# Performance work log

Measured on AMD Instinct MI355X. Metric: run time of the kernel, lower is better.

The kernel has to match this reference:

```python
import jax, jax.numpy as jnp
import numpy as np


def setup_inputs() -> dict:
    key = jax.random.key(0)
    k1, k2, k3, k4 = jax.random.split(key, 4)
    B, Cin, Cout, N, modes = 16, 128, 128, 8192, 64
    scale = 1.0 / (Cin * Cout)
    x = jax.random.normal(k1, (B, Cin, N), dtype=jnp.float32)
    # spectral weight: [in, out, modes, 2] uniform in [0, scale) like torch.rand * scale
    w_spec = scale * jax.random.uniform(k2, (Cin, Cout, modes, 2), dtype=jnp.float32)
    # Conv1d(kernel=1) weight [out, in] and bias [out] (kaiming-uniform-ish init)
    bound = 1.0 / np.sqrt(Cin)
    w_conv = jax.random.uniform(k3, (Cout, Cin), minval=-bound, maxval=bound, dtype=jnp.float32)
    b_conv = jax.random.uniform(k4, (Cout,), minval=-bound, maxval=bound, dtype=jnp.float32)
    return {"x": x, "w_spec": w_spec, "w_conv": w_conv, "b_conv": b_conv}


def reference(x, w_spec, w_conv, b_conv):
    N = x.shape[-1]
    modes = w_spec.shape[2]
    n_freq = N // 2 + 1
    # Spectral conv: rfft, keep first `modes` coefficients, complex channel mix
    x_ft = jnp.fft.rfft(x)  # [B, Cin, n_freq] complex64
    w_c = w_spec[..., 0] + 1j * w_spec[..., 1]  # [Cin, Cout, modes]
    out_m = jnp.einsum('bim,iom->bom', x_ft[:, :, :modes], w_c)  # [B, Cout, modes]
    out_ft = jnp.pad(out_m, ((0, 0), (0, 0), (0, n_freq - modes)))
    x1 = jnp.fft.irfft(out_ft, n=N)  # [B, Cout, N]
    # 1x1 conv (pointwise channel mix)
    x2 = jnp.einsum('bin,oi->bon', x, w_conv) + b_conv[None, :, None]
    return jax.nn.gelu(x1 + x2, approximate=False)
```

## Files before the change

kernel.cpp:

```cpp
#include <hip/hip_runtime.h>
#include <hip/hip_bf16.h>
#include <math.h>

#define NB    16
#define NCIN  128
#define NCOUT 128
#define NN    8192
#define NMOD  64

typedef short bf16x8 __attribute__((ext_vector_type(8)));
typedef float f32x4  __attribute__((ext_vector_type(4)));

#define MFMA16(a, b, c) __builtin_amdgcn_mfma_f32_16x16x32_bf16((a), (b), (c), 0, 0, 0)

__device__ inline unsigned short f2bf_rne(float f) {
    unsigned u = __float_as_uint(f);
    u += 0x7FFF + ((u >> 16) & 1);
    return (unsigned short)(u >> 16);
}
__device__ inline short f2bf_trunc(float f) {
    return (short)(__float_as_uint(f) >> 16);
}

__global__ __launch_bounds__(256) void k_prep(const float* __restrict__ wc,
                                              const float* __restrict__ wsp,
                                              unsigned short* __restrict__ T,
                                              unsigned short* __restrict__ Tt,
                                              unsigned short* __restrict__ Wcb,
                                              unsigned short* __restrict__ Wpk) {
    const float C = 7.66990393943e-4f;
    if (blockIdx.x < 16) {
        int a = blockIdx.x * 256 + threadIdx.x;
        int k = a >> 6, n0 = (a & 63) * 128;
        for (int j8 = 0; j8 < 16; ++j8) {
            short c8[8], s8[8];
            #pragma unroll
            for (int j = 0; j < 8; ++j) {
                int n = n0 + j8 * 8 + j;
                int ph = (k * n) & (NN - 1);
                float sn, cs; __sincosf((float)ph * C, &sn, &cs);
                c8[j] = (short)f2bf_rne(cs);
                s8[j] = (short)f2bf_rne(-sn);
            }
            *(bf16x8*)(T + (size_t)(2 * k) * NN + n0 + j8 * 8)     = *(bf16x8*)c8;
            *(bf16x8*)(T + (size_t)(2 * k + 1) * NN + n0 + j8 * 8) = *(bf16x8*)s8;
        }
    } else if (blockIdx.x < 48) {
        int n = (blockIdx.x - 16) * 256 + threadIdx.x;
        for (int k4 = 0; k4 < 16; ++k4) {
            short buf[8];
            #pragma unroll
            for (int j = 0; j < 4; ++j) {
                int k = k4 * 4 + j;
                int ph = (n * k) & (NN - 1);
                float sn, cs; __sincosf((float)ph * C, &sn, &cs);
                buf[2 * j]     = (short)f2bf_rne(cs);
                buf[2 * j + 1] = (short)f2bf_rne(-sn);
            }
            *(bf16x8*)(Tt + (size_t)n * 128 + k4 * 8) = *(bf16x8*)buf;
        }
    } else if (blockIdx.x < 112) {
        int j = (blockIdx.x - 48) * 256 + threadIdx.x;
        if (j < NCOUT * NCIN) Wcb[j] = f2bf_rne(wc[j]);
    } else {
        int g2 = (blockIdx.x - 112) * 256 + threadIdx.x;
        int k  = g2 & 63;
        int o  = (g2 >> 6) & 127;
        int ch = g2 >> 13;
        const float s = (k == 0) ? (1.f / NN) : (2.f / NN);
        const float2* wp = (const float2*)wsp;
        unsigned short* wre = Wpk + ((size_t)(k * 2 + 0) * 128 + o) * 256;
        unsigned short* wim = Wpk + ((size_t)(k * 2 + 1) * 128 + o) * 256;
        for (int c = ch * 8; c < ch * 8 + 8; ++c) {
            int i0 = 4 * c;
            short re8[8], im8[8];
            #pragma unroll
            for (int t2 = 0; t2 < 4; ++t2) {
                float2 wv = wp[((size_t)(i0 + t2) * 128 + o) * 64 + k];
                float wr = s * wv.x, wi = s * wv.y;
                re8[2 * t2]     = (short)f2bf_rne(wr);
                re8[2 * t2 + 1] = (short)f2bf_rne(-wi);
                im8[2 * t2]     = (k == 0) ? (short)0 : (short)f2bf_rne(wi);
                im8[2 * t2 + 1] = (k == 0) ? (short)0 : (short)f2bf_rne(wr);
            }
            *(bf16x8*)(wre + c * 8) = *(bf16x8*)re8;
            *(bf16x8*)(wim + c * 8) = *(bf16x8*)im8;
        }
    }
}

__global__ __launch_bounds__(256) void k_dftmm(const float* __restrict__ x,
                                               const unsigned short* __restrict__ T,
                                               float* __restrict__ Cpart) {
    const int mt = blockIdx.x & 63, sp = blockIdx.x >> 6;
    const int w = threadIdx.x >> 6, l = threadIdx.x & 63;
    const int l15 = l & 15, q = l >> 4;
    const int colbase = w * 32;
    __shared__ short As[8192];

    const int sr = threadIdx.x >> 3;
    const int sc = threadIdx.x & 7;
    const float* xrow = x + (size_t)(mt * 32 + sr) * NN + sp * 512 + sc * 16;
    short* wp0 = As + sr * 128 + (((sc * 2    ) ^ (sr & 7)) * 8);
    short* wp1 = As + sr * 128 + (((sc * 2 + 1) ^ (sr & 7)) * 8);

    float4 ra, rb, rc, rd;
#define LOADC(c) { const float* p_ = xrow + (c) * 128;                         \
        ra = *(const float4*)p_;       rb = *(const float4*)(p_ + 4);          \
        rc = *(const float4*)(p_ + 8); rd = *(const float4*)(p_ + 12); }
#define WRITEC(bufi) {                                                          \
        short t0_[8] = { f2bf_trunc(ra.x), f2bf_trunc(ra.y), f2bf_trunc(ra.z), f2bf_trunc(ra.w), \
                         f2bf_trunc(rb.x), f2bf_trunc(rb.y), f2bf_trunc(rb.z), f2bf_trunc(rb.w) }; \
        short t1_[8] = { f2bf_trunc(rc.x), f2bf_trunc(rc.y), f2bf_trunc(rc.z), f2bf_trunc(rc.w), \
                         f2bf_trunc(rd.x), f2bf_trunc(rd.y), f2bf_trunc(rd.z), f2bf_trunc(rd.w) }; \
        *(bf16x8*)(wp0 + (bufi) * 4096) = *(bf16x8*)t0_;                        \
        *(bf16x8*)(wp1 + (bufi) * 4096) = *(bf16x8*)t1_; }

    const unsigned short* Tp0 = T + (size_t)(colbase + l15) * NN + sp * 512 + q * 8;
    const unsigned short* Tp1 = Tp0 + (size_t)16 * NN;

    const int rsw = l15 & 7;

    LOADC(0);
    WRITEC(0);
    __syncthreads();

    f32x4 acc[2][2] = {};
    int buf = 0;
    for (int c = 0; c < 4; ++c) {
        if (c < 3) LOADC(c + 1);
        const short* Ab = As + buf * 4096;
        #pragma unroll
        for (int kk = 0; kk < 4; ++kk) {
            int ce = ((kk * 4 + q) ^ rsw) * 8;
            bf16x8 a0 = *(const bf16x8*)(Ab + l15 * 128 + ce);
            bf16x8 a1 = *(const bf16x8*)(Ab + (16 + l15) * 128 + ce);
            bf16x8 b0 = *(const bf16x8*)(Tp0 + c * 128 + kk * 32);
            bf16x8 b1 = *(const bf16x8*)(Tp1 + c * 128 + kk * 32);
            acc[0][0] = MFMA16(a0, b0, acc[0][0]);
            acc[0][1] = MFMA16(a0, b1, acc[0][1]);
            acc[1][0] = MFMA16(a1, b0, acc[1][0]);
            acc[1][1] = MFMA16(a1, b1, acc[1][1]);
        }
        if (c < 3) {
            WRITEC(buf ^ 1);
            __syncthreads();
            buf ^= 1;
        }
    }
#undef LOADC
#undef WRITEC

    #pragma unroll
    for (int mf = 0; mf < 2; ++mf)
        #pragma unroll
        for (int nf = 0; nf < 2; ++nf) {
            int col  = colbase + nf * 16 + l15;
            int row0 = mt * 32 + mf * 16 + q * 4;
            *(f32x4*)(Cpart + (size_t)sp * 262144 + (size_t)col * 2048 + row0) = acc[mf][nf];
        }
}

__global__ __launch_bounds__(256) void k_reduce(const float* __restrict__ Cpart,
                                                float* __restrict__ Xf) {
    int t = blockIdx.x * 256 + threadIdx.x;
    float s = 0.f;
    #pragma unroll
    for (int sp = 0; sp < 16; ++sp) s += Cpart[(size_t)sp * 262144 + t];
    Xf[t] = s;
}

__global__ __launch_bounds__(64) void k_mixmm(const float* __restrict__ Xf,
                                              const unsigned short* __restrict__ Wpk,
                                              unsigned short* __restrict__ Aspec) {
    const int k = blockIdx.x >> 3, oq = blockIdx.x & 7;
    const int l = threadIdx.x, l15 = l & 15, q = l >> 4;
    f32x4 ar = {}, ai = {};
    const float* xr = Xf + (size_t)(2 * k) * 2048 + l15 * 128;
    const float* xi = xr + 2048;
    const int o = oq * 16 + l15;
    #pragma unroll
    for (int kt = 0; kt < 8; ++kt) {
        int i0 = kt * 16 + q * 4;
        float4 r4 = *(const float4*)(xr + i0);
        float4 i4 = *(const float4*)(xi + i0);
        short a8[8] = { (short)f2bf_rne(r4.x), (short)f2bf_rne(i4.x),
                        (short)f2bf_rne(r4.y), (short)f2bf_rne(i4.y),
                        (short)f2bf_rne(r4.z), (short)f2bf_rne(i4.z),
                        (short)f2bf_rne(r4.w), (short)f2bf_rne(i4.w) };
        bf16x8 a = *(bf16x8*)a8;
        const unsigned short* wb = Wpk + ((size_t)(k * 2) * 128 + o) * 256 + kt * 32 + q * 8;
        bf16x8 bre = *(const bf16x8*)wb;
        bf16x8 bim = *(const bf16x8*)(wb + 32768);
        ar = MFMA16(a, bre, ar);
        ai = MFMA16(a, bim, ai);
    }
    #pragma unroll
    for (int r = 0; r < 4; ++r) {
        int b = q * 4 + r;
        unsigned v = (unsigned)f2bf_rne(ar[r]) | ((unsigned)f2bf_rne(ai[r]) << 16);
        *(unsigned*)(Aspec + ((size_t)b * 128 + o) * 128 + 2 * k) = v;
    }
}

__global__ __launch_bounds__(256) void k_out(const float* __restrict__ x,
                                             const unsigned short* __restrict__ Tt,
                                             const unsigned short* __restrict__ Aspec,
                                             const unsigned short* __restrict__ Wcb,
                                             const float* __restrict__ bias,
                                             float* __restrict__ out) {
    const int b = blockIdx.x >> 7, nt = blockIdx.x & 127;
    const int w = threadIdx.x >> 6, l = threadIdx.x & 63;
    const int l15 = l & 15, q = l >> 4;
    const int wo = w >> 1, wn = w & 1;
    __shared__ short xs[8192];

    const float* xb = x + (size_t)b * 128 * NN + nt * 64;
    #pragma unroll
    for (int it = 0; it < 4; ++it) {
        int unit = it * 256 + threadIdx.x;
        int ipair = unit >> 4, nq = unit & 15;
        int i0 = ipair * 2;
        const float* p0 = xb + (size_t)i0 * NN + nq * 4;
        float4 r0 = *(const float4*)p0;
        float4 r1 = *(const float4*)(p0 + NN);
        float a0[4] = { r0.x, r0.y, r0.z, r0.w };
        float a1[4] = { r1.x, r1.y, r1.z, r1.w };
        #pragma unroll
        for (int j = 0; j < 4; ++j) {
            int n = nq * 4 + j;
            unsigned v = (unsigned)(unsigned short)f2bf_trunc(a0[j])
                       | ((unsigned)(unsigned short)f2bf_trunc(a1[j]) << 16);
            int swz = (n ^ (n >> 2)) & 15;
            int addr = n * 128 + (((i0 >> 3) ^ swz) * 8) + (i0 & 7);
            *(unsigned*)&xs[addr] = v;
        }
    }

    const int obase = wo * 64;
    const int nbase = nt * 64 + wn * 32;
    f32x4 acc[4][2] = {};
    #pragma unroll
    for (int kt = 0; kt < 4; ++kt) {
        bf16x8 bb[2];
        #pragma unroll
        for (int nf = 0; nf < 2; ++nf) {
            int n = nbase + nf * 16 + l15;
            bb[nf] = *(const bf16x8*)(Tt + (size_t)n * 128 + kt * 32 + q * 8);
        }
        const unsigned short* Ap = Aspec + (size_t)b * 16384 + kt * 32 + q * 8;
        #pragma unroll
        for (int mf = 0; mf < 4; ++mf) {
            bf16x8 a = *(const bf16x8*)(Ap + (size_t)(obase + mf * 16 + l15) * 128);
            acc[mf][0] = MFMA16(a, bb[0], acc[mf][0]);
            acc[mf][1] = MFMA16(a, bb[1], acc[mf][1]);
        }
    }
    __syncthreads();
    #pragma unroll
    for (int kt = 0; kt < 4; ++kt) {
        bf16x8 bb[2];
        #pragma unroll
        for (int nf = 0; nf < 2; ++nf) {
            int nl = wn * 32 + nf * 16 + l15;
            int c  = kt * 4 + q;
            int swz = (nl ^ (nl >> 2)) & 15;
            bb[nf] = *(const bf16x8*)&xs[nl * 128 + ((c ^ swz) * 8)];
        }
        const unsigned short* Ap = Wcb + kt * 32 + q * 8;
        #pragma unroll
        for (int mf = 0; mf < 4; ++mf) {
            bf16x8 a = *(const bf16x8*)(Ap + (size_t)(obase + mf * 16 + l15) * 128);
            acc[mf][0] = MFMA16(a, bb[0], acc[mf][0]);
            acc[mf][1] = MFMA16(a, bb[1], acc[mf][1]);
        }
    }
    #pragma unroll
    for (int mf = 0; mf < 4; ++mf)
        #pragma unroll
        for (int nf = 0; nf < 2; ++nf)
            #pragma unroll
            for (int r = 0; r < 4; ++r) {
                int o = obase + mf * 16 + q * 4 + r;
                int n = nbase + nf * 16 + l15;
                float v = acc[mf][nf][r] + bias[o];
                float u = v * v;
                float p = v * fmaf(0.0713548162f, u, 1.5957691216f);
                float e = __expf(-p);
                float g = v * __builtin_amdgcn_rcpf(1.f + e);
                out[((size_t)(b * 128 + o)) * NN + n] = g;
            }
}

extern "C" void kernel_launch(void* const* d_in, const int* in_sizes, int n_in,
                              void* d_out, int out_size, void* d_ws, size_t ws_size,
                              hipStream_t stream) {
    const float* x    = (const float*)d_in[0];
    const float* wsp  = (const float*)d_in[1];
    const float* wc   = (const float*)d_in[2];
    const float* bc   = (const float*)d_in[3];
    float* out = (float*)d_out;

    unsigned short* T   = (unsigned short*)d_ws;
    unsigned short* Tt  = T + (size_t)1048576;
    unsigned short* Wcb = Tt + (size_t)1048576;
    unsigned short* Asp = Wcb + 16384;
    unsigned short* Wpk = Asp + 262144;
    float* Cpart = (float*)(Wpk + (size_t)8388608);
    float* Xf    = Cpart + (size_t)16 * 262144;

    k_prep  <<<240,  256, 0, stream>>>(wc, wsp, T, Tt, Wcb, Wpk);
    k_dftmm <<<1024, 256, 0, stream>>>(x, T, Cpart);
    k_reduce<<<1024, 256, 0, stream>>>(Cpart, Xf);
    k_mixmm <<<512,  64,  0, stream>>>(Xf, Wpk, Asp);
    k_out   <<<2048, 256, 0, stream>>>(x, Tt, Asp, Wcb, bc, out);
}
```

Measured before the change: 197.9 us.

## Transpose DFT partials layout, pre-pack bf16 in reduce, halve output tile

k_dftmm now writes its partial sums in row-major [row][col] scalar stores instead of transposed f32x4 stores. k_reduce converts the summed spectrum to bf16 and stores it already interleaved in the MFMA A-operand order, so k_mixmm can load the operand with one vector load instead of converting floats. k_out uses 32-column tiles with each wave owning 32 output channels, which doubles the block count and halves the shared-memory footprint. The tradeoffs are scattered scalar stores in k_dftmm and k_reduce, and more blocks in k_out that each reload the spectral and conv weights.

```diff
diff --git a/kernel.cpp b/kernel.cpp
--- a/kernel.cpp
+++ b/kernel.cpp
@@ -155,40 +155,38 @@
     for (int mf = 0; mf < 2; ++mf)
         #pragma unroll
         for (int nf = 0; nf < 2; ++nf) {
-            int col  = colbase + nf * 16 + l15;
-            int row0 = mt * 32 + mf * 16 + q * 4;
-            *(f32x4*)(Cpart + (size_t)sp * 262144 + (size_t)col * 2048 + row0) = acc[mf][nf];
+            int col = colbase + nf * 16 + l15;
+            #pragma unroll
+            for (int r = 0; r < 4; ++r) {
+                int row = mt * 32 + mf * 16 + q * 4 + r;
+                Cpart[(size_t)sp * 262144 + (size_t)row * 128 + col] = acc[mf][nf][r];
+            }
         }
 }
 
 __global__ __launch_bounds__(256) void k_reduce(const float* __restrict__ Cpart,
-                                                float* __restrict__ Xf) {
+                                                unsigned short* __restrict__ Axh) {
     int t = blockIdx.x * 256 + threadIdx.x;
     float s = 0.f;
     #pragma unroll
     for (int sp = 0; sp < 16; ++sp) s += Cpart[(size_t)sp * 262144 + t];
-    Xf[t] = s;
-}
-
-__global__ __launch_bounds__(64) void k_mixmm(const float* __restrict__ Xf,
+    int col = t & 127, row = t >> 7;
+    int k = col >> 1, p = col & 1;
+    int b = row >> 7, i = row & 127;
+    Axh[((size_t)k * 16 + b) * 256 + i * 2 + p] = f2bf_rne(s);
+}
+
+__global__ __launch_bounds__(64) void k_mixmm(const unsigned short* __restrict__ Axh,
                                               const unsigned short* __restrict__ Wpk,
                                               unsigned short* __restrict__ Aspec) {
     const int k = blockIdx.x >> 3, oq = blockIdx.x & 7;
     const int l = threadIdx.x, l15 = l & 15, q = l >> 4;
     f32x4 ar = {}, ai = {};
-    const float* xr = Xf + (size_t)(2 * k) * 2048 + l15 * 128;
-    const float* xi = xr + 2048;
+    const unsigned short* Ab = Axh + ((size_t)k * 16 + l15) * 256;
     const int o = oq * 16 + l15;
     #pragma unroll
     for (int kt = 0; kt < 8; ++kt) {
-        int i0 = kt * 16 + q * 4;
-        float4 r4 = *(const float4*)(xr + i0);
-        float4 i4 = *(const float4*)(xi + i0);
-        short a8[8] = { (short)f2bf_rne(r4.x), (short)f2bf_rne(i4.x),
-                        (short)f2bf_rne(r4.y), (short)f2bf_rne(i4.y),
-                        (short)f2bf_rne(r4.z), (short)f2bf_rne(i4.z),
-                        (short)f2bf_rne(r4.w), (short)f2bf_rne(i4.w) };
-        bf16x8 a = *(bf16x8*)a8;
+        bf16x8 a = *(const bf16x8*)(Ab + kt * 32 + q * 8);
         const unsigned short* wb = Wpk + ((size_t)(k * 2) * 128 + o) * 256 + kt * 32 + q * 8;
         bf16x8 bre = *(const bf16x8*)wb;
         bf16x8 bim = *(const bf16x8*)(wb + 32768);
@@ -209,17 +207,16 @@
                                              const unsigned short* __restrict__ Wcb,
                                              const float* __restrict__ bias,
                                              float* __restrict__ out) {
-    const int b = blockIdx.x >> 7, nt = blockIdx.x & 127;
+    const int b = blockIdx.x >> 8, nt = blockIdx.x & 255;
     const int w = threadIdx.x >> 6, l = threadIdx.x & 63;
     const int l15 = l & 15, q = l >> 4;
-    const int wo = w >> 1, wn = w & 1;
-    __shared__ short xs[8192];
-
-    const float* xb = x + (size_t)b * 128 * NN + nt * 64;
-    #pragma unroll
-    for (int it = 0; it < 4; ++it) {
+    __shared__ short xs[4096];
+
+    const float* xb = x + (size_t)b * 128 * NN + nt * 32;
+    #pragma unroll
+    for (int it = 0; it < 2; ++it) {
         int unit = it * 256 + threadIdx.x;
-        int ipair = unit >> 4, nq = unit & 15;
+        int ipair = unit >> 3, nq = unit & 7;
         int i0 = ipair * 2;
         const float* p0 = xb + (size_t)i0 * NN + nq * 4;
         float4 r0 = *(const float4*)p0;
@@ -237,9 +234,9 @@
         }
     }
 
-    const int obase = wo * 64;
-    const int nbase = nt * 64 + wn * 32;
-    f32x4 acc[4][2] = {};
+    const int obase = w * 32;
+    const int nbase = nt * 32;
+    f32x4 acc[2][2] = {};
     #pragma unroll
     for (int kt = 0; kt < 4; ++kt) {
         bf16x8 bb[2];
@@ -250,7 +247,7 @@
         }
         const unsigned short* Ap = Aspec + (size_t)b * 16384 + kt * 32 + q * 8;
         #pragma unroll
-        for (int mf = 0; mf < 4; ++mf) {
+        for (int mf = 0; mf < 2; ++mf) {
             bf16x8 a = *(const bf16x8*)(Ap + (size_t)(obase + mf * 16 + l15) * 128);
             acc[mf][0] = MFMA16(a, bb[0], acc[mf][0]);
             acc[mf][1] = MFMA16(a, bb[1], acc[mf][1]);
@@ -262,21 +259,21 @@
         bf16x8 bb[2];
         #pragma unroll
         for (int nf = 0; nf < 2; ++nf) {
-            int nl = wn * 32 + nf * 16 + l15;
+            int nl = nf * 16 + l15;
             int c  = kt * 4 + q;
             int swz = (nl ^ (nl >> 2)) & 15;
             bb[nf] = *(const bf16x8*)&xs[nl * 128 + ((c ^ swz) * 8)];
         }
         const unsigned short* Ap = Wcb + kt * 32 + q * 8;
         #pragma unroll
-        for (int mf = 0; mf < 4; ++mf) {
+        for (int mf = 0; mf < 2; ++mf) {
             bf16x8 a = *(const bf16x8*)(Ap + (size_t)(obase + mf * 16 + l15) * 128);
             acc[mf][0] = MFMA16(a, bb[0], acc[mf][0]);
             acc[mf][1] = MFMA16(a, bb[1], acc[mf][1]);
         }
     }
     #pragma unroll
-    for (int mf = 0; mf < 4; ++mf)
+    for (int mf = 0; mf < 2; ++mf)
         #pragma unroll
         for (int nf = 0; nf < 2; ++nf)
             #pragma unroll
@@ -307,11 +304,11 @@
     unsigned short* Asp = Wcb + 16384;
     unsigned short* Wpk = Asp + 262144;
     float* Cpart = (float*)(Wpk + (size_t)8388608);
-    float* Xf    = Cpart + (size_t)16 * 262144;
+    unsigned short* Axh = (unsigned short*)(Cpart + (size_t)16 * 262144);
 
     k_prep  <<<240,  256, 0, stream>>>(wc, wsp, T, Tt, Wcb, Wpk);
     k_dftmm <<<1024, 256, 0, stream>>>(x, T, Cpart);
-    k_reduce<<<1024, 256, 0, stream>>>(Cpart, Xf);
-    k_mixmm <<<512,  64,  0, stream>>>(Xf, Wpk, Asp);
-    k_out   <<<2048, 256, 0, stream>>>(x, Tt, Asp, Wcb, bc, out);
-}
+    k_reduce<<<1024, 256, 0, stream>>>(Cpart, Axh);
+    k_mixmm <<<512,  64,  0, stream>>>(Axh, Wpk, Asp);
+    k_out   <<<4096, 256, 0, stream>>>(x, Tt, Asp, Wcb, bc, out);
+}
```

New measurement: 204.1 us. 3.1% more time.
